# Performance work log

Measured on AMD Instinct MI355X. Metric: run time of the kernel, lower is better.

## Reference

```python
import jax, jax.numpy as jnp
import numpy as np


def masked_softmax(x, m, axis):
    # x clamped, multiplicatively masked before and after exp (faithful to source)
    x = jnp.clip(x, -15.0, 15.0)
    x = x * m
    e_x = jnp.exp(x - jnp.max(x, axis=axis, keepdims=True))
    e_x = e_x * m
    return e_x / (jnp.sum(e_x, axis=axis, keepdims=True) + 1e-6)


def setup_inputs() -> dict:
    key = jax.random.key(0)
    kC, kQ, kcm, kqm, kwC, kwQ, kwm = jax.random.split(key, 7)
    B, Lc, Lq, d = 16, 1024, 256, 512
    C = jax.random.normal(kC, (B, Lc, d), dtype=jnp.float32)
    Q = jax.random.normal(kQ, (B, Lq, d), dtype=jnp.float32)
    Cmask = jax.random.randint(kcm, (B, Lc), 0, 2, dtype=jnp.int32)
    Qmask = jax.random.randint(kqm, (B, Lq), 0, 2, dtype=jnp.int32)
    # xavier_uniform bound for shape (d, 1): sqrt(6/(d+1))
    bnd = float(np.sqrt(6.0 / (d + 1)))
    w4C = jax.random.uniform(kwC, (d, 1), jnp.float32, -bnd, bnd)
    w4Q = jax.random.uniform(kwQ, (d, 1), jnp.float32, -bnd, bnd)
    bnd_m = float(np.sqrt(6.0 / (1 + d)))
    w4mlu = jax.random.uniform(kwm, (1, 1, d), jnp.float32, -bnd_m, bnd_m)
    bias = jnp.zeros((1,), dtype=jnp.float32)
    return {"C": C, "Q": Q, "Cmask": Cmask, "Qmask": Qmask,
            "w4C": w4C, "w4Q": w4Q, "w4mlu": w4mlu, "bias": bias}


def reference(C, Q, Cmask, Qmask, w4C, w4Q, w4mlu, bias):
    # trilinear similarity S: [B, Lc, Lq]
    sub0 = jnp.matmul(C, w4C)                      # [B, Lc, 1]
    sub1 = jnp.swapaxes(jnp.matmul(Q, w4Q), 1, 2)  # [B, 1, Lq]
    sub2 = jnp.matmul(C * w4mlu, jnp.swapaxes(Q, 1, 2))  # [B, Lc, Lq]
    S = sub0 + sub1 + sub2 + bias

    Cm = Cmask.astype(jnp.float32)[:, :, None]  # [B, Lc, 1]
    Qm = Qmask.astype(jnp.float32)[:, None, :]  # [B, 1, Lq]
    S1 = masked_softmax(S, Qm, axis=2)  # rows over question
    S2 = masked_softmax(S, Cm, axis=1)  # cols over context

    A = jnp.matmul(S1, Q)                                   # [B, Lc, d]
    Bt = jnp.matmul(jnp.matmul(S1, jnp.swapaxes(S2, 1, 2)), C)  # [B, Lc, d]
    return jnp.concatenate([C, A, C * A, C * Bt], axis=2)   # [B, Lc, 4d]
```

## Files before the change

kernel.cpp:

```cpp
#include <hip/hip_runtime.h>
#include <cstdint>
#include <cstddef>


typedef __attribute__((ext_vector_type(8))) short short8;
typedef __attribute__((ext_vector_type(4))) short short4v;
typedef __attribute__((ext_vector_type(4))) float f32x4;
typedef __attribute__((ext_vector_type(8))) __bf16 bf16x8;

__device__ __forceinline__ short f2bf(float f) {
  unsigned u = __builtin_bit_cast(unsigned, f);
  u += 0x7fffu + ((u >> 16) & 1u);
  return (short)(u >> 16);
}

__device__ __forceinline__ void gload16(const void* g, void* l) {
  __builtin_amdgcn_global_load_lds(
      (const __attribute__((address_space(1))) void*)g,
      (__attribute__((address_space(3))) void*)l, 16, 0, 0);
}

__device__ __forceinline__ f32x4 mfma16(short8 a, short8 b, f32x4 c) {
  return __builtin_amdgcn_mfma_f32_16x16x32_bf16(
      __builtin_bit_cast(bf16x8, a), __builtin_bit_cast(bf16x8, b), c, 0, 0, 0);
}

__device__ __forceinline__ short8 pack8(float4 x, float4 y) {
  short8 s;
  s[0] = f2bf(x.x); s[1] = f2bf(x.y); s[2] = f2bf(x.z); s[3] = f2bf(x.w);
  s[4] = f2bf(y.x); s[5] = f2bf(y.y); s[6] = f2bf(y.z); s[7] = f2bf(y.w);
  return s;
}
__device__ __forceinline__ float dot4(float4 a, float4 b) {
  return a.x * b.x + a.y * b.y + a.z * b.z + a.w * b.w;
}


__global__ __launch_bounds__(256) void prep_tr(const float* __restrict__ C,
                                               const float* __restrict__ Q,
                                               short* __restrict__ Ctb,
                                               short* __restrict__ QT) {
  __shared__ short tile[32][33];
  const int bz = blockIdx.z;
  const bool isC = blockIdx.y < 32;
  const int ry = isC ? blockIdx.y : blockIdx.y - 32;
  const int R = isC ? 1024 : 256;
  const float* ip = isC ? C + (size_t)bz * 1024 * 512
                        : Q + (size_t)bz * 256 * 512;
  short* op = isC ? Ctb + (size_t)bz * 512 * 1024
                  : QT + (size_t)bz * 1024 * 256;
  const int c0 = blockIdx.x * 32, r0 = ry * 32;
  const int tx = threadIdx.x & 31, ty = threadIdx.x >> 5;
#pragma unroll
  for (int i = 0; i < 32; i += 8)
    tile[ty + i][tx] = f2bf(ip[(size_t)(r0 + ty + i) * 512 + c0 + tx]);
  __syncthreads();
#pragma unroll
  for (int i = 0; i < 32; i += 8)
    op[(size_t)(c0 + ty + i) * R + r0 + tx] = tile[tx][ty + i];
}


__device__ __forceinline__ void gemm_core(const short* __restrict__ A,
                                          const short* __restrict__ B, int K,
                                          int lda, int ldb, int m0, int n0,
                                          short* ldsA, short* ldsB,
                                          f32x4 (&acc)[4][4]) {
  const int tid = threadIdx.x;
  const int lane = tid & 63;
  const int wave = tid >> 6;
  const int wr = (wave >> 1) * 64, wc = (wave & 1) * 64;
  const int fr = lane & 15;
  const int fk = (lane >> 4) * 8;
  const int srow = tid >> 2;
  const int skoff = (tid & 3) * 8;

  const short* Ag = A + (size_t)(m0 + srow) * lda + skoff;
  const short* Ag2 = A + (size_t)(m0 + 64 + srow) * lda + skoff;
  const short* Bg = B + (size_t)(n0 + srow) * ldb + skoff;
  const short* Bg2 = B + (size_t)(n0 + 64 + srow) * ldb + skoff;
  short* la = ldsA + tid * 8;
  short* la2 = ldsA + 64 * 32 + tid * 8;
  short* lb = ldsB + tid * 8;
  short* lb2 = ldsB + 64 * 32 + tid * 8;

  for (int k0 = 0; k0 < K; k0 += 32) {
    gload16(Ag + k0, la);
    gload16(Ag2 + k0, la2);
    gload16(Bg + k0, lb);
    gload16(Bg2 + k0, lb2);
    __syncthreads();
    short8 af[4], bf[4];
#pragma unroll
    for (int m = 0; m < 4; ++m)
      af[m] = *(const short8*)(ldsA + (wr + m * 16 + fr) * 32 + fk);
#pragma unroll
    for (int n = 0; n < 4; ++n)
      bf[n] = *(const short8*)(ldsB + (wc + n * 16 + fr) * 32 + fk);
#pragma unroll
    for (int m = 0; m < 4; ++m)
#pragma unroll
      for (int n = 0; n < 4; ++n) acc[m][n] = mfma16(af[m], bf[n], acc[m][n]);
    __syncthreads();
  }
}

#define GEMM_PROLOGUE()                                        \
  __shared__ __attribute__((aligned(16))) short ldsA[128 * 32];\
  __shared__ __attribute__((aligned(16))) short ldsB[128 * 32];\
  const int b = blockIdx.z;                                    \
  const int m0 = blockIdx.x * 128, n0 = blockIdx.y * 128;      \
  f32x4 acc[4][4];                                             \
  {                                                            \
    f32x4 z = {0.f, 0.f, 0.f, 0.f};                            \
    _Pragma("unroll") for (int m = 0; m < 4; ++m)              \
        _Pragma("unroll") for (int n = 0; n < 4; ++n) acc[m][n] = z; \
  }                                                            \
  const int lane = threadIdx.x & 63, wave = threadIdx.x >> 6;  \
  const int wr = (wave >> 1) * 64, wc = (wave & 1) * 64;       \
  const int cr = (lane >> 4) * 4, cc = lane & 15;


__global__ __launch_bounds__(256) void gemm_S_fused(
    const float* __restrict__ C, const float* __restrict__ Q,
    const int* __restrict__ Qmask, const int* __restrict__ Cmask,
    const float* __restrict__ w4C, const float* __restrict__ w4Q,
    const float* __restrict__ w4mlu, const float* __restrict__ bias,
    short* __restrict__ S1, short* __restrict__ Eu,
    float* __restrict__ partial) {
  __shared__ __attribute__((aligned(16))) char smem_raw[256 * 72 * 2];
  short* ldsA = (short*)smem_raw;
  short* ldsB = (short*)(smem_raw + 64 * 32 * 2);
  short* eT = (short*)smem_raw;
  __shared__ float sub0_l[64];
  __shared__ float sub1_l[256];
  __shared__ float redS[4][64];

  const int b = blockIdx.y;
  const int m0 = blockIdx.x * 64;
  const int tid = threadIdx.x;
  const int lane = tid & 63, wave = tid >> 6;

  const float* Cb = C + ((size_t)b * 1024 + m0) * 512;
  const float* Qb = Q + (size_t)b * 256 * 512;

  const int srow = tid >> 2;
  const int skk = (tid & 3) * 8;

  f32x4 acc[4][4];
  {
    f32x4 z = {0.f, 0.f, 0.f, 0.f};
#pragma unroll
    for (int m = 0; m < 4; ++m)
#pragma unroll
      for (int n = 0; n < 4; ++n) acc[m][n] = z;
  }
  float dotA = 0.f;
  float dotB[4] = {0.f, 0.f, 0.f, 0.f};

  const int fr = lane & 15, fk = (lane >> 4) * 8;

  for (int k0 = 0; k0 < 512; k0 += 32) {
    float4 a0 = *(const float4*)(Cb + (size_t)srow * 512 + k0 + skk);
    float4 a1 = *(const float4*)(Cb + (size_t)srow * 512 + k0 + skk + 4);
    float4 q0[4], q1[4];
#pragma unroll
    for (int r4 = 0; r4 < 4; ++r4) {
      const float* qp = Qb + (size_t)(srow + 64 * r4) * 512 + k0 + skk;
      q0[r4] = *(const float4*)qp;
      q1[r4] = *(const float4*)(qp + 4);
    }
    float4 wm0 = *(const float4*)(w4mlu + k0 + skk);
    float4 wm1 = *(const float4*)(w4mlu + k0 + skk + 4);
    float4 wc0 = *(const float4*)(w4C + k0 + skk);
    float4 wc1 = *(const float4*)(w4C + k0 + skk + 4);
    float4 wq0 = *(const float4*)(w4Q + k0 + skk);
    float4 wq1 = *(const float4*)(w4Q + k0 + skk + 4);

    dotA += dot4(a0, wc0) + dot4(a1, wc1);
#pragma unroll
    for (int r4 = 0; r4 < 4; ++r4)
      dotB[r4] += dot4(q0[r4], wq0) + dot4(q1[r4], wq1);

    float4 am0, am1;
    am0.x = a0.x * wm0.x; am0.y = a0.y * wm0.y;
    am0.z = a0.z * wm0.z; am0.w = a0.w * wm0.w;
    am1.x = a1.x * wm1.x; am1.y = a1.y * wm1.y;
    am1.z = a1.z * wm1.z; am1.w = a1.w * wm1.w;
    short8 as = pack8(am0, am1);
    short8 bs[4];
#pragma unroll
    for (int r4 = 0; r4 < 4; ++r4) bs[r4] = pack8(q0[r4], q1[r4]);

    __syncthreads();
    *(short8*)(ldsA + srow * 32 + skk) = as;
#pragma unroll
    for (int r4 = 0; r4 < 4; ++r4)
      *(short8*)(ldsB + (srow + 64 * r4) * 32 + skk) = bs[r4];
    __syncthreads();

    short8 af[4], bfv[4];
#pragma unroll
    for (int m = 0; m < 4; ++m)
      af[m] = *(const short8*)(ldsA + (m * 16 + fr) * 32 + fk);
#pragma unroll
    for (int n = 0; n < 4; ++n)
      bfv[n] = *(const short8*)(ldsB + (wave * 64 + n * 16 + fr) * 32 + fk);
#pragma unroll
    for (int m = 0; m < 4; ++m)
#pragma unroll
      for (int n = 0; n < 4; ++n) acc[m][n] = mfma16(af[m], bfv[n], acc[m][n]);
  }

  dotA += __shfl_xor(dotA, 1, 64);
  dotA += __shfl_xor(dotA, 2, 64);
#pragma unroll
  for (int r4 = 0; r4 < 4; ++r4) {
    dotB[r4] += __shfl_xor(dotB[r4], 1, 64);
    dotB[r4] += __shfl_xor(dotB[r4], 2, 64);
  }
  if ((tid & 3) == 0) {
    sub0_l[srow] = dotA;
#pragma unroll
    for (int r4 = 0; r4 < 4; ++r4) sub1_l[srow + 64 * r4] = dotB[r4];
  }
  __syncthreads();

  const float bv = bias[0];
  const int cc = lane & 15, cr = (lane >> 4) * 4;
  float qmv[4];
#pragma unroll
  for (int n = 0; n < 4; ++n)
    qmv[n] = (float)Qmask[b * 256 + wave * 64 + n * 16 + cc];
  float cmv[4][4];
#pragma unroll
  for (int m = 0; m < 4; ++m)
#pragma unroll
    for (int i = 0; i < 4; ++i)
      cmv[m][i] = (float)Cmask[b * 1024 + m0 + m * 16 + cr + i];

#pragma unroll
  for (int m = 0; m < 4; ++m)
#pragma unroll
    for (int n = 0; n < 4; ++n)
#pragma unroll
      for (int i = 0; i < 4; ++i) {
        float v = acc[m][n][i] + sub0_l[m * 16 + cr + i] +
                  sub1_l[wave * 64 + n * 16 + cc] + bv;
        acc[m][n][i] = fminf(15.f, fmaxf(-15.f, v));
      }

  float ps[4] = {0.f, 0.f, 0.f, 0.f};
#pragma unroll
  for (int m = 0; m < 4; ++m)
#pragma unroll
    for (int n = 0; n < 4; ++n) {
      short4v o;
#pragma unroll
      for (int i = 0; i < 4; ++i) {
        float cm = cmv[m][i];
        float ec = cm * __expf(acc[m][n][i] * cm - 8.f);
        ps[n] += ec;
        o[i] = f2bf(ec);
      }
      *(short4v*)(eT + (wave * 64 + n * 16 + cc) * 72 + m * 16 + cr) = o;
    }
#pragma unroll
  for (int n = 0; n < 4; ++n) {
    ps[n] += __shfl_xor(ps[n], 16, 64);
    ps[n] += __shfl_xor(ps[n], 32, 64);
  }
  if (lane < 16) {
#pragma unroll
    for (int n = 0; n < 4; ++n)
      partial[((size_t)b * 16 + blockIdx.x) * 256 + wave * 64 + n * 16 + cc] =
          ps[n];
  }
  __syncthreads();

  short* Eub = Eu + (size_t)b * 262144 + m0;
#pragma unroll
  for (int it = 0; it < 8; ++it) {
    int q = it * 32 + wave * 8 + (lane >> 3);
    int k = lane & 7;
    short8 v = *(const short8*)(eT + q * 72 + k * 8);
    *(short8*)(Eub + (size_t)q * 1024 + k * 8) = v;
  }

  float rs[4][4];
#pragma unroll
  for (int m = 0; m < 4; ++m)
#pragma unroll
    for (int i = 0; i < 4; ++i) {
      rs[m][i] = 0.f;
#pragma unroll
      for (int n = 0; n < 4; ++n) {
        float eq = qmv[n] * __expf(acc[m][n][i] * qmv[n] - 8.f);
        acc[m][n][i] = eq;
        rs[m][i] += eq;
      }
    }
#pragma unroll
  for (int m = 0; m < 4; ++m)
#pragma unroll
    for (int i = 0; i < 4; ++i) {
      rs[m][i] += __shfl_xor(rs[m][i], 1, 64);
      rs[m][i] += __shfl_xor(rs[m][i], 2, 64);
      rs[m][i] += __shfl_xor(rs[m][i], 4, 64);
      rs[m][i] += __shfl_xor(rs[m][i], 8, 64);
    }
  if (cc == 0) {
#pragma unroll
    for (int m = 0; m < 4; ++m)
#pragma unroll
      for (int i = 0; i < 4; ++i) redS[wave][m * 16 + cr + i] = rs[m][i];
  }
  __syncthreads();

  short* S1b = S1 + (size_t)b * 262144 + (size_t)m0 * 256;
#pragma unroll
  for (int m = 0; m < 4; ++m)
#pragma unroll
    for (int i = 0; i < 4; ++i) {
      int r = m * 16 + cr + i;
      float sum = redS[0][r] + redS[1][r] + redS[2][r] + redS[3][r];
      float inv = 1.f / (sum + 1e-6f);
#pragma unroll
      for (int n = 0; n < 4; ++n)
        S1b[(size_t)r * 256 + wave * 64 + n * 16 + cc] =
            f2bf(acc[m][n][i] * inv);
    }
}


__global__ __launch_bounds__(256) void gemm_T2(const short* __restrict__ Ctb,
                                               const short* __restrict__ Eu,
                                               const float* __restrict__ partial,
                                               short* __restrict__ QTbot) {
  GEMM_PROLOGUE();
  gemm_core(Ctb + (size_t)b * 512 * 1024, Eu + (size_t)b * 256 * 1024, 1024,
            1024, 1024, m0, n0, ldsA, ldsB, acc);
  const float* pb = partial + (size_t)b * 16 * 256;
  float invv[4];
#pragma unroll
  for (int n = 0; n < 4; ++n) {
    int c = n0 + wc + n * 16 + cc;
    float s = 0.f;
#pragma unroll
    for (int k = 0; k < 16; ++k) s += pb[k * 256 + c];
    invv[n] = 1.f / (s + 1e-6f);
  }
  short* Tp = QTbot + (size_t)b * (1024 * 256);
#pragma unroll
  for (int m = 0; m < 4; ++m)
#pragma unroll
    for (int n = 0; n < 4; ++n)
#pragma unroll
      for (int i = 0; i < 4; ++i) {
        int r = m0 + wr + m * 16 + cr + i;
        int c = n0 + wc + n * 16 + cc;
        Tp[(size_t)r * 256 + c] = f2bf(acc[m][n][i] * invv[n]);
      }
}


__global__ __launch_bounds__(256) void gemm_AB(const short* __restrict__ S1,
                                               const short* __restrict__ QT,
                                               const float* __restrict__ C,
                                               float* __restrict__ out) {
  GEMM_PROLOGUE();
  gemm_core(S1 + (size_t)b * 1024 * 256, QT + (size_t)b * 1024 * 256, 256, 256,
            256, m0, n0, ldsA, ldsB, acc);
  const bool topHalf = (n0 < 512);
#pragma unroll
  for (int m = 0; m < 4; ++m)
#pragma unroll
    for (int n = 0; n < 4; ++n)
#pragma unroll
      for (int i = 0; i < 4; ++i) {
        int r = m0 + wr + m * 16 + cr + i;
        int c = n0 + wc + n * 16 + cc;
        float a = acc[m][n][i];
        size_t base = ((size_t)b * 1024 + r) * 2048;
        if (topHalf) {
          float cv = C[((size_t)b * 1024 + r) * 512 + c];
          __builtin_nontemporal_store(cv, &out[base + c]);
          __builtin_nontemporal_store(a, &out[base + 512 + c]);
          __builtin_nontemporal_store(cv * a, &out[base + 1024 + c]);
        } else {
          int c2 = c - 512;
          float cv = C[((size_t)b * 1024 + r) * 512 + c2];
          __builtin_nontemporal_store(cv * a, &out[base + 1536 + c2]);
        }
      }
}


extern "C" void kernel_launch(void* const* d_in, const int* in_sizes, int n_in,
                              void* d_out, int out_size, void* d_ws,
                              size_t ws_size, hipStream_t stream) {
  const float* C = (const float*)d_in[0];
  const float* Q = (const float*)d_in[1];
  const int* Cmask = (const int*)d_in[2];
  const int* Qmask = (const int*)d_in[3];
  const float* w4C = (const float*)d_in[4];
  const float* w4Q = (const float*)d_in[5];
  const float* w4mlu = (const float*)d_in[6];
  const float* bias = (const float*)d_in[7];
  float* out = (float*)d_out;

  size_t off = 0;
  auto alloc = [&](size_t n) {
    void* p = (char*)d_ws + off;
    off += (n + 255) & ~(size_t)255;
    return p;
  };
  short* Ctb = (short*)alloc((size_t)16 * 512 * 1024 * 2);
  short* QT = (short*)alloc((size_t)16 * 1024 * 256 * 2);
  short* S1 = (short*)alloc((size_t)16 * 1024 * 256 * 2);
  short* Eu = (short*)alloc((size_t)16 * 256 * 1024 * 2);
  float* partial = (float*)alloc((size_t)16 * 16 * 256 * 4);

  prep_tr<<<dim3(16, 40, 16), dim3(256), 0, stream>>>(C, Q, Ctb, QT);
  gemm_S_fused<<<dim3(16, 16), dim3(256), 0, stream>>>(
      C, Q, Qmask, Cmask, w4C, w4Q, w4mlu, bias, S1, Eu, partial);
  gemm_T2<<<dim3(4, 2, 16), dim3(256), 0, stream>>>(Ctb, Eu, partial,
                                                    QT + (size_t)512 * 256);
  gemm_AB<<<dim3(8, 8, 16), dim3(256), 0, stream>>>(S1, QT, C, out);
}
```

Measured before the change: 127.9 us.

## Merge independent kernels into heterogeneous launches to overlap prep, S, T2 and AB-top

Folds the transpose/convert prep work into the same launch as the fused S kernel, using block-index ranges to pick the role, with wider 64x64 float4 transpose tiles. It also runs the top half of the A/B output GEMM (which needs only Q^T and S1) in the same launch as the T2 GEMM, which now uses smaller 64x64 tiles to raise block count. The bottom half of the output GEMM runs last. The aim is to cut launch gaps and tail underutilisation by overlapping independent stages, at the cost of mixed-shape blocks sharing one launch and its LDS/register budget.

```diff
diff --git a/kernel.cpp b/kernel.cpp
--- a/kernel.cpp
+++ b/kernel.cpp
@@ -33,31 +33,6 @@
 }
 __device__ __forceinline__ float dot4(float4 a, float4 b) {
   return a.x * b.x + a.y * b.y + a.z * b.z + a.w * b.w;
-}
-
-
-__global__ __launch_bounds__(256) void prep_tr(const float* __restrict__ C,
-                                               const float* __restrict__ Q,
-                                               short* __restrict__ Ctb,
-                                               short* __restrict__ QT) {
-  __shared__ short tile[32][33];
-  const int bz = blockIdx.z;
-  const bool isC = blockIdx.y < 32;
-  const int ry = isC ? blockIdx.y : blockIdx.y - 32;
-  const int R = isC ? 1024 : 256;
-  const float* ip = isC ? C + (size_t)bz * 1024 * 512
-                        : Q + (size_t)bz * 256 * 512;
-  short* op = isC ? Ctb + (size_t)bz * 512 * 1024
-                  : QT + (size_t)bz * 1024 * 256;
-  const int c0 = blockIdx.x * 32, r0 = ry * 32;
-  const int tx = threadIdx.x & 31, ty = threadIdx.x >> 5;
-#pragma unroll
-  for (int i = 0; i < 32; i += 8)
-    tile[ty + i][tx] = f2bf(ip[(size_t)(r0 + ty + i) * 512 + c0 + tx]);
-  __syncthreads();
-#pragma unroll
-  for (int i = 0; i < 32; i += 8)
-    op[(size_t)(c0 + ty + i) * R + r0 + tx] = tile[tx][ty + i];
 }
 
 
@@ -105,39 +80,82 @@
   }
 }
 
-#define GEMM_PROLOGUE()                                        \
-  __shared__ __attribute__((aligned(16))) short ldsA[128 * 32];\
-  __shared__ __attribute__((aligned(16))) short ldsB[128 * 32];\
-  const int b = blockIdx.z;                                    \
-  const int m0 = blockIdx.x * 128, n0 = blockIdx.y * 128;      \
-  f32x4 acc[4][4];                                             \
-  {                                                            \
-    f32x4 z = {0.f, 0.f, 0.f, 0.f};                            \
-    _Pragma("unroll") for (int m = 0; m < 4; ++m)              \
-        _Pragma("unroll") for (int n = 0; n < 4; ++n) acc[m][n] = z; \
-  }                                                            \
-  const int lane = threadIdx.x & 63, wave = threadIdx.x >> 6;  \
-  const int wr = (wave >> 1) * 64, wc = (wave & 1) * 64;       \
-  const int cr = (lane >> 4) * 4, cc = lane & 15;
-
-
-__global__ __launch_bounds__(256) void gemm_S_fused(
+__device__ __forceinline__ void gemm_core64(const short* __restrict__ A,
+                                            const short* __restrict__ B, int K,
+                                            int lda, int ldb, int m0, int n0,
+                                            short* ldsA, short* ldsB,
+                                            f32x4 (&acc)[2][2]) {
+  const int tid = threadIdx.x;
+  const int lane = tid & 63;
+  const int wave = tid >> 6;
+  const int wr = (wave >> 1) * 32, wc = (wave & 1) * 32;
+  const int fr = lane & 15;
+  const int fk = (lane >> 4) * 8;
+  const int srow = tid >> 2;
+  const int skoff = (tid & 3) * 8;
+
+  const short* Ag = A + (size_t)(m0 + srow) * lda + skoff;
+  const short* Bg = B + (size_t)(n0 + srow) * ldb + skoff;
+  short* la = ldsA + tid * 8;
+  short* lb = ldsB + tid * 8;
+
+  for (int k0 = 0; k0 < K; k0 += 32) {
+    gload16(Ag + k0, la);
+    gload16(Bg + k0, lb);
+    __syncthreads();
+    short8 af[2], bf[2];
+#pragma unroll
+    for (int m = 0; m < 2; ++m)
+      af[m] = *(const short8*)(ldsA + (wr + m * 16 + fr) * 32 + fk);
+#pragma unroll
+    for (int n = 0; n < 2; ++n)
+      bf[n] = *(const short8*)(ldsB + (wc + n * 16 + fr) * 32 + fk);
+#pragma unroll
+    for (int m = 0; m < 2; ++m)
+#pragma unroll
+      for (int n = 0; n < 2; ++n) acc[m][n] = mfma16(af[m], bf[n], acc[m][n]);
+    __syncthreads();
+  }
+}
+
+
+__device__ __forceinline__ void prep_tile64(const float* __restrict__ ip,
+                                            short* __restrict__ op, int outld,
+                                            int r0, int c0, short* tile) {
+  const int tx = threadIdx.x & 15, ty = threadIdx.x >> 4;
+#pragma unroll
+  for (int i = 0; i < 64; i += 16) {
+    float4 v = *(const float4*)(ip + (size_t)(r0 + ty + i) * 512 + c0 + tx * 4);
+    short* t = tile + (ty + i) * 66 + tx * 4;
+    t[0] = f2bf(v.x); t[1] = f2bf(v.y); t[2] = f2bf(v.z); t[3] = f2bf(v.w);
+  }
+  __syncthreads();
+#pragma unroll
+  for (int i = 0; i < 64; i += 16) {
+    const int orow = ty + i, ocol = tx * 4;
+    short4v o;
+#pragma unroll
+    for (int j = 0; j < 4; ++j) o[j] = tile[(ocol + j) * 66 + orow];
+    *(short4v*)(op + (size_t)(c0 + orow) * outld + r0 + ocol) = o;
+  }
+}
+
+
+__device__ __forceinline__ void s_fused_body(
     const float* __restrict__ C, const float* __restrict__ Q,
     const int* __restrict__ Qmask, const int* __restrict__ Cmask,
     const float* __restrict__ w4C, const float* __restrict__ w4Q,
     const float* __restrict__ w4mlu, const float* __restrict__ bias,
     short* __restrict__ S1, short* __restrict__ Eu,
-    float* __restrict__ partial) {
-  __shared__ __attribute__((aligned(16))) char smem_raw[256 * 72 * 2];
-  short* ldsA = (short*)smem_raw;
-  short* ldsB = (short*)(smem_raw + 64 * 32 * 2);
-  short* eT = (short*)smem_raw;
-  __shared__ float sub0_l[64];
-  __shared__ float sub1_l[256];
-  __shared__ float redS[4][64];
-
-  const int b = blockIdx.y;
-  const int m0 = blockIdx.x * 64;
+    float* __restrict__ partial, int b, int mblk, char* sm) {
+  short* ldsA = (short*)sm;
+  short* ldsB = (short*)(sm + 64 * 32 * 2);
+  short* eT = (short*)sm;
+  float* sub0_l = (float*)(sm + 36864);
+  float* sub1_l = (float*)(sm + 37120);
+  float(*redS)[64] = (float(*)[64])(sm + 38144);
+
+  const int m0 = mblk * 64;
   const int tid = threadIdx.x;
   const int lane = tid & 63, wave = tid >> 6;
 
@@ -273,8 +291,7 @@
   if (lane < 16) {
 #pragma unroll
     for (int n = 0; n < 4; ++n)
-      partial[((size_t)b * 16 + blockIdx.x) * 256 + wave * 64 + n * 16 + cc] =
-          ps[n];
+      partial[((size_t)b * 16 + mblk) * 256 + wave * 64 + n * 16 + cc] = ps[n];
   }
   __syncthreads();
 
@@ -333,65 +350,143 @@
 }
 
 
-__global__ __launch_bounds__(256) void gemm_T2(const short* __restrict__ Ctb,
-                                               const short* __restrict__ Eu,
-                                               const float* __restrict__ partial,
-                                               short* __restrict__ QTbot) {
-  GEMM_PROLOGUE();
-  gemm_core(Ctb + (size_t)b * 512 * 1024, Eu + (size_t)b * 256 * 1024, 1024,
-            1024, 1024, m0, n0, ldsA, ldsB, acc);
-  const float* pb = partial + (size_t)b * 16 * 256;
-  float invv[4];
-#pragma unroll
-  for (int n = 0; n < 4; ++n) {
-    int c = n0 + wc + n * 16 + cc;
-    float s = 0.f;
-#pragma unroll
-    for (int k = 0; k < 16; ++k) s += pb[k * 256 + c];
-    invv[n] = 1.f / (s + 1e-6f);
-  }
-  short* Tp = QTbot + (size_t)b * (1024 * 256);
-#pragma unroll
-  for (int m = 0; m < 4; ++m)
-#pragma unroll
-    for (int n = 0; n < 4; ++n)
-#pragma unroll
-      for (int i = 0; i < 4; ++i) {
-        int r = m0 + wr + m * 16 + cr + i;
-        int c = n0 + wc + n * 16 + cc;
-        Tp[(size_t)r * 256 + c] = f2bf(acc[m][n][i] * invv[n]);
-      }
-}
-
-
-__global__ __launch_bounds__(256) void gemm_AB(const short* __restrict__ S1,
-                                               const short* __restrict__ QT,
-                                               const float* __restrict__ C,
-                                               float* __restrict__ out) {
-  GEMM_PROLOGUE();
-  gemm_core(S1 + (size_t)b * 1024 * 256, QT + (size_t)b * 1024 * 256, 256, 256,
-            256, m0, n0, ldsA, ldsB, acc);
-  const bool topHalf = (n0 < 512);
-#pragma unroll
-  for (int m = 0; m < 4; ++m)
-#pragma unroll
-    for (int n = 0; n < 4; ++n)
-#pragma unroll
-      for (int i = 0; i < 4; ++i) {
-        int r = m0 + wr + m * 16 + cr + i;
-        int c = n0 + wc + n * 16 + cc;
-        float a = acc[m][n][i];
-        size_t base = ((size_t)b * 1024 + r) * 2048;
-        if (topHalf) {
-          float cv = C[((size_t)b * 1024 + r) * 512 + c];
+__global__ __launch_bounds__(256) void stage1(
+    const float* __restrict__ C, const float* __restrict__ Q,
+    const int* __restrict__ Qmask, const int* __restrict__ Cmask,
+    const float* __restrict__ w4C, const float* __restrict__ w4Q,
+    const float* __restrict__ w4mlu, const float* __restrict__ bias,
+    short* __restrict__ S1, short* __restrict__ Eu,
+    float* __restrict__ partial, short* __restrict__ Ctb,
+    short* __restrict__ QT) {
+  __shared__ __attribute__((aligned(16))) char sm[39168];
+  const int id = blockIdx.x;
+  if (id < 256) {
+    s_fused_body(C, Q, Qmask, Cmask, w4C, w4Q, w4mlu, bias, S1, Eu, partial,
+                 id >> 4, id & 15, sm);
+  } else if (id < 2304) {
+    const int p = id - 256, b = p >> 7, t = p & 127;
+    prep_tile64(C + (size_t)b * 1024 * 512, Ctb + (size_t)b * 512 * 1024, 1024,
+                (t >> 3) * 64, (t & 7) * 64, (short*)sm);
+  } else {
+    const int p = id - 2304, b = p >> 5, t = p & 31;
+    prep_tile64(Q + (size_t)b * 256 * 512, QT + (size_t)b * 1024 * 256, 256,
+                (t >> 3) * 64, (t & 7) * 64, (short*)sm);
+  }
+}
+
+
+__global__ __launch_bounds__(256) void stage2(
+    const short* __restrict__ Ctb, const short* __restrict__ Eu,
+    const float* __restrict__ partial, short* __restrict__ QT,
+    const short* __restrict__ S1, const float* __restrict__ C,
+    float* __restrict__ out) {
+  __shared__ __attribute__((aligned(16))) char sm[16384];
+  short* ldsA = (short*)sm;
+  short* ldsB = (short*)(sm + 8192);
+  const int id = blockIdx.x;
+  const int lane = threadIdx.x & 63, wave = threadIdx.x >> 6;
+  const int cr = (lane >> 4) * 4, cc = lane & 15;
+
+  if (id < 512) {
+    const int b = id >> 5, r = id & 31;
+    const int m0 = (r >> 2) * 128, n0 = (r & 3) * 128;
+    const int wr = (wave >> 1) * 64, wc = (wave & 1) * 64;
+    f32x4 acc[4][4];
+    {
+      f32x4 z = {0.f, 0.f, 0.f, 0.f};
+#pragma unroll
+      for (int m = 0; m < 4; ++m)
+#pragma unroll
+        for (int n = 0; n < 4; ++n) acc[m][n] = z;
+    }
+    gemm_core(S1 + (size_t)b * 1024 * 256, QT + (size_t)b * 1024 * 256, 256,
+              256, 256, m0, n0, ldsA, ldsB, acc);
+#pragma unroll
+    for (int m = 0; m < 4; ++m)
+#pragma unroll
+      for (int n = 0; n < 4; ++n)
+#pragma unroll
+        for (int i = 0; i < 4; ++i) {
+          int rr = m0 + wr + m * 16 + cr + i;
+          int c = n0 + wc + n * 16 + cc;
+          float a = acc[m][n][i];
+          float cv = C[((size_t)b * 1024 + rr) * 512 + c];
+          size_t base = ((size_t)b * 1024 + rr) * 2048;
           __builtin_nontemporal_store(cv, &out[base + c]);
           __builtin_nontemporal_store(a, &out[base + 512 + c]);
           __builtin_nontemporal_store(cv * a, &out[base + 1024 + c]);
-        } else {
-          int c2 = c - 512;
-          float cv = C[((size_t)b * 1024 + r) * 512 + c2];
-          __builtin_nontemporal_store(cv * a, &out[base + 1536 + c2]);
         }
+  } else {
+    const int t = id - 512, b = t >> 5, r = t & 31;
+    const int m0 = (r >> 2) * 64, n0 = (r & 3) * 64;
+    const int wr = (wave >> 1) * 32, wc = (wave & 1) * 32;
+    f32x4 acc[2][2];
+    {
+      f32x4 z = {0.f, 0.f, 0.f, 0.f};
+#pragma unroll
+      for (int m = 0; m < 2; ++m)
+#pragma unroll
+        for (int n = 0; n < 2; ++n) acc[m][n] = z;
+    }
+    gemm_core64(Ctb + (size_t)b * 512 * 1024, Eu + (size_t)b * 256 * 1024,
+                1024, 1024, 1024, m0, n0, ldsA, ldsB, acc);
+    const float* pb = partial + (size_t)b * 16 * 256;
+    float invv[2];
+#pragma unroll
+    for (int n = 0; n < 2; ++n) {
+      int c = n0 + wc + n * 16 + cc;
+      float s = 0.f;
+#pragma unroll
+      for (int k = 0; k < 16; ++k) s += pb[k * 256 + c];
+      invv[n] = 1.f / (s + 1e-6f);
+    }
+    short* Tp = QT + (size_t)b * 1024 * 256 + 512 * 256;
+#pragma unroll
+    for (int m = 0; m < 2; ++m)
+#pragma unroll
+      for (int n = 0; n < 2; ++n)
+#pragma unroll
+        for (int i = 0; i < 4; ++i) {
+          int rr = m0 + wr + m * 16 + cr + i;
+          int c = n0 + wc + n * 16 + cc;
+          Tp[(size_t)rr * 256 + c] = f2bf(acc[m][n][i] * invv[n]);
+        }
+  }
+}
+
+
+__global__ __launch_bounds__(256) void gemm_ABbot(const short* __restrict__ S1,
+                                                  const short* __restrict__ QT,
+                                                  const float* __restrict__ C,
+                                                  float* __restrict__ out) {
+  __shared__ __attribute__((aligned(16))) short ldsA[128 * 32];
+  __shared__ __attribute__((aligned(16))) short ldsB[128 * 32];
+  const int b = blockIdx.z;
+  const int m0 = blockIdx.x * 128, n0 = 512 + blockIdx.y * 128;
+  f32x4 acc[4][4];
+  {
+    f32x4 z = {0.f, 0.f, 0.f, 0.f};
+#pragma unroll
+    for (int m = 0; m < 4; ++m)
+#pragma unroll
+      for (int n = 0; n < 4; ++n) acc[m][n] = z;
+  }
+  const int lane = threadIdx.x & 63, wave = threadIdx.x >> 6;
+  const int wr = (wave >> 1) * 64, wc = (wave & 1) * 64;
+  const int cr = (lane >> 4) * 4, cc = lane & 15;
+  gemm_core(S1 + (size_t)b * 1024 * 256, QT + (size_t)b * 1024 * 256, 256, 256,
+            256, m0, n0, ldsA, ldsB, acc);
+#pragma unroll
+  for (int m = 0; m < 4; ++m)
+#pragma unroll
+    for (int n = 0; n < 4; ++n)
+#pragma unroll
+      for (int i = 0; i < 4; ++i) {
+        int rr = m0 + wr + m * 16 + cr + i;
+        int cq = (n0 - 512) + wc + n * 16 + cc;
+        float cv = C[((size_t)b * 1024 + rr) * 512 + cq];
+        size_t base = ((size_t)b * 1024 + rr) * 2048;
+        __builtin_nontemporal_store(cv * acc[m][n][i], &out[base + 1536 + cq]);
       }
 }
 
@@ -421,10 +516,10 @@
   short* Eu = (short*)alloc((size_t)16 * 256 * 1024 * 2);
   float* partial = (float*)alloc((size_t)16 * 16 * 256 * 4);
 
-  prep_tr<<<dim3(16, 40, 16), dim3(256), 0, stream>>>(C, Q, Ctb, QT);
-  gemm_S_fused<<<dim3(16, 16), dim3(256), 0, stream>>>(
-      C, Q, Qmask, Cmask, w4C, w4Q, w4mlu, bias, S1, Eu, partial);
-  gemm_T2<<<dim3(4, 2, 16), dim3(256), 0, stream>>>(Ctb, Eu, partial,
-                                                    QT + (size_t)512 * 256);
-  gemm_AB<<<dim3(8, 8, 16), dim3(256), 0, stream>>>(S1, QT, C, out);
-}
+  stage1<<<dim3(2816), dim3(256), 0, stream>>>(C, Q, Qmask, Cmask, w4C, w4Q,
+                                               w4mlu, bias, S1, Eu, partial,
+                                               Ctb, QT);
+  stage2<<<dim3(1024), dim3(256), 0, stream>>>(Ctb, Eu, partial, QT, S1, C,
+                                               out);
+  gemm_ABbot<<<dim3(8, 4, 16), dim3(256), 0, stream>>>(S1, QT, C, out);
+}
```

Result: faster. 105.5 us, median of 2 (-17.5%).
